# Kernel tuning notes

Measured on AMD Instinct MI355X. Metric: run time of the kernel, lower is better.

## Reference

```python
import jax, jax.numpy as jnp
import numpy as np
from jax import lax

INPUT_DIM = 4
HIDDEN_DIM = 32
PRED_STEPS = 50
BATCH = 32768
SEQ_LEN = 200


def setup_inputs() -> dict:
    key = jax.random.key(0)
    ks = jax.random.split(key, 7)
    s = 1.0 / np.sqrt(HIDDEN_DIM)  # PyTorch LSTM init scale
    return {
        "history_data": jax.random.normal(ks[0], (BATCH, SEQ_LEN, INPUT_DIM), dtype=jnp.float32),
        "W_ih": jax.random.uniform(ks[1], (4 * HIDDEN_DIM, INPUT_DIM), jnp.float32, -s, s),
        "W_hh": jax.random.uniform(ks[2], (4 * HIDDEN_DIM, HIDDEN_DIM), jnp.float32, -s, s),
        "b_ih": jax.random.uniform(ks[3], (4 * HIDDEN_DIM,), jnp.float32, -s, s),
        "b_hh": jax.random.uniform(ks[4], (4 * HIDDEN_DIM,), jnp.float32, -s, s),
        "W_pred": jax.random.uniform(ks[5], (INPUT_DIM, HIDDEN_DIM), jnp.float32, -s, s),
        "b_pred": jax.random.uniform(ks[6], (INPUT_DIM,), jnp.float32, -s, s),
    }


def reference(history_data, W_ih, W_hh, b_ih, b_hh, W_pred, b_pred):
    H = W_hh.shape[1]
    b = b_ih + b_hh

    def cell(h, c, x):
        # PyTorch gate order: input, forget, cell(g), output
        gates = x @ W_ih.T + h @ W_hh.T + b  # [B, 4H]
        i, f, g, o = jnp.split(gates, 4, axis=-1)
        c_new = jax.nn.sigmoid(f) * c + jax.nn.sigmoid(i) * jnp.tanh(g)
        h_new = jax.nn.sigmoid(o) * jnp.tanh(c_new)
        return h_new, c_new

    B = history_data.shape[0]
    h0 = jnp.zeros((B, H), history_data.dtype)
    c0 = jnp.zeros((B, H), history_data.dtype)

    # Encode history: scan over time
    xs = jnp.swapaxes(history_data, 0, 1)  # [T, B, D]

    def hist_step(carry, x):
        h, c = carry
        h, c = cell(h, c, x)
        return (h, c), None

    (h, _), _ = lax.scan(hist_step, (h0, c0), xs)

    # each step (torch.zeros_like), carrying only h.
    def dec_step(h, _):
        pred = h @ W_pred.T + b_pred  # [B, INPUT_DIM]
        h_new, _ = cell(h, jnp.zeros_like(h), pred)
        return h_new, pred

    _, preds = lax.scan(dec_step, h, None, length=PRED_STEPS)  # [P, B, D]
    return jnp.swapaxes(preds, 0, 1)  # [B, PRED_STEPS, D]
```

## Files before the change

kernel.cpp:

```cpp
#include <hip/hip_runtime.h>
#include <math.h>

#define BATCH 32768
#define SEQLEN 200
#define PSTEPS 50
#define HID 32
#define LDS_PAD 36

typedef __attribute__((ext_vector_type(2))) _Float16 half2v;
typedef __attribute__((ext_vector_type(8))) _Float16 half8v;
typedef __attribute__((ext_vector_type(2))) __fp16   fp16x2;
typedef __attribute__((ext_vector_type(4))) float floatx4;

#define EXP2 __builtin_amdgcn_exp2f
#define RCPF __builtin_amdgcn_rcpf
#define PKRTZ __builtin_amdgcn_cvt_pkrtz

#define L1C 1.4426950408889634f
#define L2C 2.8853900817779268f

union H8 { unsigned int u[4]; half8v h; half2v h2[4]; };
union HU { fp16x2 h; unsigned int u; };

__device__ __forceinline__ unsigned int pk(float a, float b) {
    HU t; t.h = PKRTZ(a, b); return t.u;
}

__device__ __forceinline__ void lds_barrier() {
    asm volatile("s_waitcnt lgkmcnt(0)" ::: "memory");
    __builtin_amdgcn_s_barrier();
    asm volatile("" ::: "memory");
}

__global__ __launch_bounds__(128, 4)
void lstm_mfma_kernel(const float* __restrict__ hist, const float* __restrict__ W_ih,
                      const float* __restrict__ W_hh, const float* __restrict__ b_ih,
                      const float* __restrict__ b_hh, const float* __restrict__ W_pred,
                      const float* __restrict__ b_pred, float* __restrict__ out)
{
    const int lane = threadIdx.x & 63;
    const int half = threadIdx.x >> 6;
    const int m    = lane & 15;
    const int quad = lane >> 4;
    const int elem0 = blockIdx.x * 16;

    __shared__ __align__(16) float hbuf[2][16][LDS_PAD];

    half8v Bh[4], B2[4];
    #pragma unroll
    for (int g = 0; g < 4; ++g) {
        const int gc = g * 32 + half * 16 + m;
        H8 bh;
        #pragma unroll
        for (int jj = 0; jj < 4; ++jj) {
            bh.h2[jj] = (half2v){ (_Float16)W_hh[gc * HID + quad * 8 + 2 * jj],
                                  (_Float16)W_hh[gc * HID + quad * 8 + 2 * jj + 1] };
        }
        Bh[g] = bh.h;
        H8 b2; b2.u[0] = b2.u[1] = b2.u[2] = b2.u[3] = 0u;
        if (quad == 0) {
            b2.h2[0] = (half2v){ (_Float16)W_ih[gc * 4 + 0], (_Float16)W_ih[gc * 4 + 1] };
            b2.h2[1] = (half2v){ (_Float16)W_ih[gc * 4 + 2], (_Float16)W_ih[gc * 4 + 3] };
            float bsum = b_ih[gc] + b_hh[gc];
            _Float16 bhi = (_Float16)bsum;
            _Float16 blo = (_Float16)(bsum - (float)bhi);
            b2.h2[2] = (half2v){ bhi, blo };
        }
        B2[g] = b2.h;
    }
    const unsigned int one2 = 0x3C003C00u;

    float cst[4];
    #pragma unroll
    for (int r = 0; r < 4; ++r) { cst[r] = 0.f; hbuf[0][quad * 4 + r][half * 16 + m] = 0.f; }
    lds_barrier();

    const float4* xp = (const float4*)(hist + (size_t)(elem0 + m) * (SEQLEN * 4));
    float4 xv = xp[0];
    #pragma unroll 1
    for (int t = 0; t < SEQLEN; ++t) {
        const int rd = t & 1;
        float4 h0 = *(const float4*)&hbuf[rd][m][quad * 8];
        float4 h1 = *(const float4*)&hbuf[rd][m][quad * 8 + 4];
        H8 ahu;
        ahu.u[0] = pk(h0.x, h0.y); ahu.u[1] = pk(h0.z, h0.w);
        ahu.u[2] = pk(h1.x, h1.y); ahu.u[3] = pk(h1.z, h1.w);
        const half8v ah = ahu.h;

        const unsigned int tx0 = pk(xv.x, xv.y), tx1 = pk(xv.z, xv.w);
        H8 a2u;
        a2u.u[0] = (quad == 0) ? tx0 : 0u;
        a2u.u[1] = (quad == 0) ? tx1 : 0u;
        a2u.u[2] = (quad == 0) ? one2 : 0u;
        a2u.u[3] = 0u;
        const half8v a2 = a2u.h;

        const int tn = (t + 1 < SEQLEN) ? t + 1 : SEQLEN - 1;
        float4 xn = xp[tn];

        floatx4 acc[4];
        #pragma unroll
        for (int g = 0; g < 4; ++g) {
            floatx4 a = __builtin_amdgcn_mfma_f32_16x16x32_f16(a2, B2[g], (floatx4){0.f,0.f,0.f,0.f}, 0, 0, 0);
            acc[g] = __builtin_amdgcn_mfma_f32_16x16x32_f16(ah, Bh[g], a, 0, 0, 0);
        }
        #pragma unroll
        for (int r = 0; r < 4; ++r) {
            const float gi = acc[0][r], gf = acc[1][r], gg = acc[2][r], go = acc[3][r];
            const float ei = EXP2(gi * -L1C);
            const float ef = EXP2(gf * -L1C);
            const float eo = EXP2(go * -L1C);
            const float eg = EXP2(gg * L2C);
            const float pf = 1.0f + ef;
            const float t1 = (1.0f + ei) * (1.0f + eg);
            const float num = fmaf(cst[r], t1, (eg - 1.0f) * pf);
            float cn = num * RCPF(t1 * pf);
            cn = fminf(fmaxf(cn, -30.0f), 30.0f);
            const float ec = EXP2(cn * L2C);
            const float hn = (ec - 1.0f) * RCPF((1.0f + eo) * (1.0f + ec));
            cst[r] = cn;
            hbuf[rd ^ 1][quad * 4 + r][half * 16 + m] = hn;
        }
        lds_barrier();
        xv = xn;
    }

    float wp[4][8];
    #pragma unroll
    for (int d = 0; d < 4; ++d)
        #pragma unroll
        for (int j = 0; j < 8; ++j) wp[d][j] = W_pred[d * HID + quad * 8 + j];
    float bp[4] = { b_pred[0], b_pred[1], b_pred[2], b_pred[3] };

    float* op = out + (size_t)(elem0 + m) * (PSTEPS * 4);
    #pragma unroll 1
    for (int p = 0; p < PSTEPS; ++p) {
        const int rd = p & 1;
        float4 h0 = *(const float4*)&hbuf[rd][m][quad * 8];
        float4 h1 = *(const float4*)&hbuf[rd][m][quad * 8 + 4];
        const float hv[8] = { h0.x, h0.y, h0.z, h0.w, h1.x, h1.y, h1.z, h1.w };

        float pd[4];
        #pragma unroll
        for (int d = 0; d < 4; ++d) {
            float s = 0.f;
            #pragma unroll
            for (int j = 0; j < 8; ++j) s = fmaf(hv[j], wp[d][j], s);
            s += __shfl_xor(s, 16);
            s += __shfl_xor(s, 32);
            pd[d] = s + bp[d];
        }
        if (half == 0 && quad == 0) *(float4*)(op + p * 4) = make_float4(pd[0], pd[1], pd[2], pd[3]);

        if (p + 1 < PSTEPS) {
            H8 ahu;
            ahu.u[0] = pk(hv[0], hv[1]); ahu.u[1] = pk(hv[2], hv[3]);
            ahu.u[2] = pk(hv[4], hv[5]); ahu.u[3] = pk(hv[6], hv[7]);
            const half8v ah = ahu.h;
            const unsigned int tx0 = pk(pd[0], pd[1]), tx1 = pk(pd[2], pd[3]);
            H8 a2u;
            a2u.u[0] = (quad == 0) ? tx0 : 0u;
            a2u.u[1] = (quad == 0) ? tx1 : 0u;
            a2u.u[2] = (quad == 0) ? one2 : 0u;
            a2u.u[3] = 0u;
            const half8v a2 = a2u.h;

            floatx4 acc[3];
            #pragma unroll
            for (int k = 0; k < 3; ++k) {
                const int g = (k == 0) ? 0 : k + 1;
                floatx4 a = __builtin_amdgcn_mfma_f32_16x16x32_f16(a2, B2[g], (floatx4){0.f,0.f,0.f,0.f}, 0, 0, 0);
                acc[k] = __builtin_amdgcn_mfma_f32_16x16x32_f16(ah, Bh[g], a, 0, 0, 0);
            }
            #pragma unroll
            for (int r = 0; r < 4; ++r) {
                const float gi = acc[0][r], gg = acc[1][r], go = acc[2][r];
                const float ei = EXP2(gi * -L1C);
                const float eo = EXP2(go * -L1C);
                const float eg = EXP2(gg * L2C);
                const float cn = (eg - 1.0f) * RCPF((1.0f + ei) * (1.0f + eg));
                const float ec = EXP2(cn * L2C);
                const float hn = (ec - 1.0f) * RCPF((1.0f + eo) * (1.0f + ec));
                hbuf[rd ^ 1][quad * 4 + r][half * 16 + m] = hn;
            }
            lds_barrier();
        }
    }
}

extern "C" void kernel_launch(void* const* d_in, const int* in_sizes, int n_in,
                              void* d_out, int out_size, void* d_ws, size_t ws_size,
                              hipStream_t stream) {
    const float* hist   = (const float*)d_in[0];
    const float* W_ih   = (const float*)d_in[1];
    const float* W_hh   = (const float*)d_in[2];
    const float* b_ih   = (const float*)d_in[3];
    const float* b_hh   = (const float*)d_in[4];
    const float* W_pred = (const float*)d_in[5];
    const float* b_pred = (const float*)d_in[6];
    float* out = (float*)d_out;

    const int blocks = BATCH / 16;
    lstm_mfma_kernel<<<blocks, 128, 0, stream>>>(hist, W_ih, W_hh, b_ih, b_hh,
                                                 W_pred, b_pred, out);
}
```

Baseline: 433.4 us.

## Replace exp2-based gate activations with packed rational tanh approximation

Sigmoid gates are rewritten as 0.5*tanh(x/2)+0.5, with the 0.5 folded into the fp16 weights and biases. Each tanh is evaluated as a clamped Padé rational polynomial on packed float2 FMAs, and the denominators are shared so only one reciprocal is needed per group of gates. This swaps transcendental exp2 calls on the special-function unit for packed VALU FMAs. In exchange it adds polynomial work and approximation error from clamping at ±4.

```diff
diff --git a/kernel.cpp b/kernel.cpp
--- a/kernel.cpp
+++ b/kernel.cpp
@@ -11,14 +11,11 @@
 typedef __attribute__((ext_vector_type(8))) _Float16 half8v;
 typedef __attribute__((ext_vector_type(2))) __fp16   fp16x2;
 typedef __attribute__((ext_vector_type(4))) float floatx4;
-
-#define EXP2 __builtin_amdgcn_exp2f
+typedef __attribute__((ext_vector_type(2))) float float2v;
+
 #define RCPF __builtin_amdgcn_rcpf
 #define PKRTZ __builtin_amdgcn_cvt_pkrtz
 
-#define L1C 1.4426950408889634f
-#define L2C 2.8853900817779268f
-
 union H8 { unsigned int u[4]; half8v h; half2v h2[4]; };
 union HU { fp16x2 h; unsigned int u; };
 
@@ -26,10 +23,23 @@
     HU t; t.h = PKRTZ(a, b); return t.u;
 }
 
-__device__ __forceinline__ void lds_barrier() {
-    asm volatile("s_waitcnt lgkmcnt(0)" ::: "memory");
-    __builtin_amdgcn_s_barrier();
-    asm volatile("" ::: "memory");
+__device__ __forceinline__ float2v v2(float a, float b) { return (float2v){a, b}; }
+__device__ __forceinline__ float2v pfma(float2v a, float2v b, float2v c) {
+    return __builtin_elementwise_fma(a, b, c);
+}
+
+__device__ __forceinline__ float2v tanh_pq(float2v x, float2v& q) {
+    float2v xc;
+    xc.x = fminf(fmaxf(x.x, -4.0f), 4.0f);
+    xc.y = fminf(fmaxf(x.y, -4.0f), 4.0f);
+    const float2v t = xc * xc;
+    float2v p = t + v2(378.f, 378.f);
+    p = pfma(p, t, v2(17325.f, 17325.f));
+    p = pfma(p, t, v2(135135.f, 135135.f));
+    float2v qq = pfma(t, v2(28.f, 28.f), v2(3150.f, 3150.f));
+    qq = pfma(qq, t, v2(62370.f, 62370.f));
+    q = pfma(qq, t, v2(135135.f, 135135.f));
+    return xc * p;
 }
 
 __global__ __launch_bounds__(128, 4)
@@ -43,25 +53,28 @@
     const int m    = lane & 15;
     const int quad = lane >> 4;
     const int elem0 = blockIdx.x * 16;
+    const int u    = half * 16 + m;
 
     __shared__ __align__(16) float hbuf[2][16][LDS_PAD];
 
+    const float gsc[4] = { 0.5f, 0.5f, 1.0f, 0.5f };
     half8v Bh[4], B2[4];
     #pragma unroll
     for (int g = 0; g < 4; ++g) {
-        const int gc = g * 32 + half * 16 + m;
+        const int gc = g * 32 + u;
+        const float sc = gsc[g];
         H8 bh;
         #pragma unroll
         for (int jj = 0; jj < 4; ++jj) {
-            bh.h2[jj] = (half2v){ (_Float16)W_hh[gc * HID + quad * 8 + 2 * jj],
-                                  (_Float16)W_hh[gc * HID + quad * 8 + 2 * jj + 1] };
+            bh.h2[jj] = (half2v){ (_Float16)(sc * W_hh[gc * HID + quad * 8 + 2 * jj]),
+                                  (_Float16)(sc * W_hh[gc * HID + quad * 8 + 2 * jj + 1]) };
         }
         Bh[g] = bh.h;
         H8 b2; b2.u[0] = b2.u[1] = b2.u[2] = b2.u[3] = 0u;
         if (quad == 0) {
-            b2.h2[0] = (half2v){ (_Float16)W_ih[gc * 4 + 0], (_Float16)W_ih[gc * 4 + 1] };
-            b2.h2[1] = (half2v){ (_Float16)W_ih[gc * 4 + 2], (_Float16)W_ih[gc * 4 + 3] };
-            float bsum = b_ih[gc] + b_hh[gc];
+            b2.h2[0] = (half2v){ (_Float16)(sc * W_ih[gc * 4 + 0]), (_Float16)(sc * W_ih[gc * 4 + 1]) };
+            b2.h2[1] = (half2v){ (_Float16)(sc * W_ih[gc * 4 + 2]), (_Float16)(sc * W_ih[gc * 4 + 3]) };
+            float bsum = sc * (b_ih[gc] + b_hh[gc]);
             _Float16 bhi = (_Float16)bsum;
             _Float16 blo = (_Float16)(bsum - (float)bhi);
             b2.h2[2] = (half2v){ bhi, blo };
@@ -69,11 +82,13 @@
         B2[g] = b2.h;
     }
     const unsigned int one2 = 0x3C003C00u;
+    const float2v halfc = v2(0.5f, 0.5f);
 
     float cst[4];
     #pragma unroll
-    for (int r = 0; r < 4; ++r) { cst[r] = 0.f; hbuf[0][quad * 4 + r][half * 16 + m] = 0.f; }
-    lds_barrier();
+    for (int r = 0; r < 4; ++r) { cst[r] = 0.f; hbuf[0][quad * 4 + r][u] = 0.f; }
+    asm volatile("s_waitcnt lgkmcnt(0)" ::: "memory");
+    __builtin_amdgcn_s_barrier();
 
     const float4* xp = (const float4*)(hist + (size_t)(elem0 + m) * (SEQLEN * 4));
     float4 xv = xp[0];
@@ -105,23 +120,44 @@
             acc[g] = __builtin_amdgcn_mfma_f32_16x16x32_f16(ah, Bh[g], a, 0, 0, 0);
         }
         #pragma unroll
-        for (int r = 0; r < 4; ++r) {
-            const float gi = acc[0][r], gf = acc[1][r], gg = acc[2][r], go = acc[3][r];
-            const float ei = EXP2(gi * -L1C);
-            const float ef = EXP2(gf * -L1C);
-            const float eo = EXP2(go * -L1C);
-            const float eg = EXP2(gg * L2C);
-            const float pf = 1.0f + ef;
-            const float t1 = (1.0f + ei) * (1.0f + eg);
-            const float num = fmaf(cst[r], t1, (eg - 1.0f) * pf);
-            float cn = num * RCPF(t1 * pf);
-            cn = fminf(fmaxf(cn, -30.0f), 30.0f);
-            const float ec = EXP2(cn * L2C);
-            const float hn = (ec - 1.0f) * RCPF((1.0f + eo) * (1.0f + ec));
-            cst[r] = cn;
-            hbuf[rd ^ 1][quad * 4 + r][half * 16 + m] = hn;
-        }
-        lds_barrier();
+        for (int pr = 0; pr < 2; ++pr) {
+            const int r0 = pr * 2;
+            float2v gi = v2(acc[0][r0], acc[0][r0 + 1]);
+            float2v gf = v2(acc[1][r0], acc[1][r0 + 1]);
+            float2v gg = v2(acc[2][r0], acc[2][r0 + 1]);
+            float2v go = v2(acc[3][r0], acc[3][r0 + 1]);
+            float2v cc = v2(cst[r0], cst[r0 + 1]);
+
+            float2v qi, qf, qg;
+            float2v ni = tanh_pq(gi, qi);
+            float2v nf = tanh_pq(gf, qf);
+            float2v ng = tanh_pq(gg, qg);
+            float2v q2 = qi * qf;
+            float2v Q  = q2 * qg;
+            float2v R  = v2(RCPF(Q.x), RCPF(Q.y));
+            float2v Tg = ng * (R * q2);
+            float2v Tf = nf * (R * (qi * qg));
+            float2v Ti = ni * (R * (qf * qg));
+            float2v si = pfma(Ti, halfc, halfc);
+            float2v sf = pfma(Tf, halfc, halfc);
+            float2v cn = pfma(sf, cc, si * Tg);
+
+            float2v qo, qc;
+            float2v no = tanh_pq(go, qo);
+            float2v nc = tanh_pq(cn, qc);
+            float2v Q2 = qo * qc;
+            float2v R2 = v2(RCPF(Q2.x), RCPF(Q2.y));
+            float2v To = no * (R2 * qc);
+            float2v Tc = nc * (R2 * qo);
+            float2v so = pfma(To, halfc, halfc);
+            float2v hn = so * Tc;
+
+            cst[r0] = cn.x; cst[r0 + 1] = cn.y;
+            hbuf[rd ^ 1][quad * 4 + r0][u]     = hn.x;
+            hbuf[rd ^ 1][quad * 4 + r0 + 1][u] = hn.y;
+        }
+        asm volatile("s_waitcnt lgkmcnt(0)" ::: "memory");
+        __builtin_amdgcn_s_barrier();
         xv = xn;
     }
 
@@ -173,17 +209,37 @@
                 acc[k] = __builtin_amdgcn_mfma_f32_16x16x32_f16(ah, Bh[g], a, 0, 0, 0);
             }
             #pragma unroll
-            for (int r = 0; r < 4; ++r) {
-                const float gi = acc[0][r], gg = acc[1][r], go = acc[2][r];
-                const float ei = EXP2(gi * -L1C);
-                const float eo = EXP2(go * -L1C);
-                const float eg = EXP2(gg * L2C);
-                const float cn = (eg - 1.0f) * RCPF((1.0f + ei) * (1.0f + eg));
-                const float ec = EXP2(cn * L2C);
-                const float hn = (ec - 1.0f) * RCPF((1.0f + eo) * (1.0f + ec));
-                hbuf[rd ^ 1][quad * 4 + r][half * 16 + m] = hn;
+            for (int pr = 0; pr < 2; ++pr) {
+                const int r0 = pr * 2;
+                float2v gi = v2(acc[0][r0], acc[0][r0 + 1]);
+                float2v gg = v2(acc[1][r0], acc[1][r0 + 1]);
+                float2v go = v2(acc[2][r0], acc[2][r0 + 1]);
+
+                float2v qi, qg;
+                float2v ni = tanh_pq(gi, qi);
+                float2v ng = tanh_pq(gg, qg);
+                float2v Q  = qi * qg;
+                float2v R  = v2(RCPF(Q.x), RCPF(Q.y));
+                float2v Ti = ni * (R * qg);
+                float2v Tg = ng * (R * qi);
+                float2v si = pfma(Ti, halfc, halfc);
+                float2v cn = si * Tg;
+
+                float2v qo, qc;
+                float2v no = tanh_pq(go, qo);
+                float2v nc = tanh_pq(cn, qc);
+                float2v Q2 = qo * qc;
+                float2v R2 = v2(RCPF(Q2.x), RCPF(Q2.y));
+                float2v To = no * (R2 * qc);
+                float2v Tc = nc * (R2 * qo);
+                float2v so = pfma(To, halfc, halfc);
+                float2v hn = so * Tc;
+
+                hbuf[rd ^ 1][quad * 4 + r0][u]     = hn.x;
+                hbuf[rd ^ 1][quad * 4 + r0 + 1][u] = hn.y;
             }
-            lds_barrier();
+            asm volatile("s_waitcnt lgkmcnt(0)" ::: "memory");
+            __builtin_amdgcn_s_barrier();
         }
     }
 }
```

New measurement: 561.6 us. +29.6%, slower.
